# Optimization experiments

Hardware: AMD Instinct MI355X
Metric: run time of the kernel (lower is better)

## Reference

```python
import jax, jax.numpy as jnp
import numpy as np
from jax import lax

B, L, NCH, NQ, NL, FW, NCLS = 256, 3000, 4, 8, 2, 128, 5
BN_EPS = 1e-5


def setup_inputs() -> dict:
    key = jax.random.key(0)
    ks = jax.random.split(key, 24)
    rn = lambda k, shape, s=0.05: jax.random.normal(k, shape, jnp.float32) * s
    inp = {}
    inp['x'] = jax.random.normal(ks[0], (B, NCH, L), jnp.float32)
    inp['conv1_w'] = rn(ks[1], (32, NCH, 7)); inp['conv1_b'] = rn(ks[2], (32,))
    inp['bn1_g'] = 1.0 + rn(ks[3], (32,)); inp['bn1_b'] = rn(ks[3], (32,))
    inp['conv2_w'] = rn(ks[4], (64, 32, 7)); inp['conv2_b'] = rn(ks[5], (64,))
    inp['bn2_g'] = 1.0 + rn(ks[6], (64,)); inp['bn2_b'] = rn(ks[6], (64,))
    inp['conv3_w'] = rn(ks[7], (128, 64, 7)); inp['conv3_b'] = rn(ks[8], (128,))
    inp['bn3_g'] = 1.0 + rn(ks[9], (128,)); inp['bn3_b'] = rn(ks[9], (128,))
    inp['conv4_w'] = rn(ks[10], (128, 128, 7)); inp['conv4_b'] = rn(ks[11], (128,))
    inp['bn4_g'] = 1.0 + rn(ks[12], (128,)); inp['bn4_b'] = rn(ks[12], (128,))
    inp['fc_w'] = rn(ks[13], (FW, 128)); inp['fc_b'] = rn(ks[14], (FW,))
    inp['ang_w'] = rn(ks[15], (NQ, FW)); inp['ang_b'] = rn(ks[16], (NQ,))
    # TorchLayer default init: uniform in [0, 2*pi)
    inp['qw'] = jax.random.uniform(ks[17], (NL, NQ, 3), jnp.float32, 0.0, 2.0 * np.pi)
    inp['h1_w'] = rn(ks[18], (64, NQ)); inp['h1_b'] = rn(ks[19], (64,))
    inp['h2_w'] = rn(ks[20], (NCLS, 64)); inp['h2_b'] = rn(ks[21], (NCLS,))
    return inp


def _conv1d(x, w, b):
    y = lax.conv_general_dilated(x, w, (1,), [(3, 3)], dimension_numbers=('NCH', 'OIH', 'NCH'))
    return y + b[None, :, None]


def _bn(x, g, b):  # eval-mode BN: running_mean=0, running_var=1
    inv = 1.0 / np.sqrt(1.0 + BN_EPS)
    return x * (g * inv)[None, :, None] + b[None, :, None]


def _maxpool4(x):
    return lax.reduce_window(x, -jnp.inf, lax.max, (1, 1, 4), (1, 1, 4), 'VALID')


def _apply_1q(state, U, w, batched):
    # state: (B, 2**NQ); wire 0 = most significant bit (PennyLane convention)
    bs = state.shape[0]
    st = state.reshape(bs, 2 ** w, 2, -1)
    if batched:
        new = jnp.einsum('sab,slbr->slar', U, st)
    else:
        new = jnp.einsum('ab,slbr->slar', U, st)
    return new.reshape(bs, -1)


def _apply_cnot(state, c, t):
    bs = state.shape[0]
    q1, q2 = min(c, t), max(c, t)
    s = state.reshape(bs, 2 ** q1, 2, 2 ** (q2 - q1 - 1), 2, -1)
    ci, ti = (2, 4) if c < t else (4, 2)
    c0 = lax.index_in_dim(s, 0, ci, keepdims=True)
    c1 = jnp.flip(lax.index_in_dim(s, 1, ci, keepdims=True), axis=ti)
    return jnp.concatenate([c0, c1], axis=ci).reshape(bs, -1)


def _rot_matrix(phi, th, om):
    # PennyLane Rot(phi, theta, omega) = RZ(omega) RY(theta) RZ(phi)
    cm, sm = jnp.cos(th / 2), jnp.sin(th / 2)
    m00 = jnp.exp(-0.5j * (phi + om)) * cm
    m01 = -jnp.exp(0.5j * (phi - om)) * sm
    m10 = jnp.exp(-0.5j * (phi - om)) * sm
    m11 = jnp.exp(0.5j * (phi + om)) * cm
    return jnp.stack([jnp.stack([m00, m01]), jnp.stack([m10, m11])]).astype(jnp.complex64)


def _qsim(angles, qw):
    bs = angles.shape[0]
    dim = 2 ** NQ
    state = jnp.zeros((bs, dim), jnp.complex64).at[:, 0].set(1.0)
    # AngleEmbedding: RY(angle_w) on each wire (batched matrices)
    c, s = jnp.cos(angles / 2), jnp.sin(angles / 2)
    for w in range(NQ):
        U = jnp.stack([jnp.stack([c[:, w], -s[:, w]], -1),
                       jnp.stack([s[:, w], c[:, w]], -1)], -2).astype(jnp.complex64)
        state = _apply_1q(state, U, w, batched=True)
    # StronglyEntanglingLayers: Rot on each wire, then CNOT ring with range r
    for l in range(NL):
        for w in range(NQ):
            U = _rot_matrix(qw[l, w, 0], qw[l, w, 1], qw[l, w, 2])
            state = _apply_1q(state, U, w, batched=False)
        r = (l % (NQ - 1)) + 1
        for i in range(NQ):
            state = _apply_cnot(state, i, (i + r) % NQ)
    probs = state.real ** 2 + state.imag ** 2
    z = [probs.reshape(bs, 2 ** w, 2, -1)[:, :, 0].sum((1, 2))
         - probs.reshape(bs, 2 ** w, 2, -1)[:, :, 1].sum((1, 2)) for w in range(NQ)]
    return jnp.stack(z, -1)  # (B, NQ)


def reference(x, conv1_w, conv1_b, bn1_g, bn1_b, conv2_w, conv2_b, bn2_g, bn2_b,
              conv3_w, conv3_b, bn3_g, bn3_b, conv4_w, conv4_b, bn4_g, bn4_b,
              fc_w, fc_b, ang_w, ang_b, qw, h1_w, h1_b, h2_w, h2_b):
    h = jax.nn.relu(_bn(_conv1d(x, conv1_w, conv1_b), bn1_g, bn1_b))
    h = jax.nn.relu(_bn(_conv1d(h, conv2_w, conv2_b), bn2_g, bn2_b))
    h = _maxpool4(h)
    h = jax.nn.relu(_bn(_conv1d(h, conv3_w, conv3_b), bn3_g, bn3_b))
    h = _maxpool4(h)
    h = jax.nn.relu(_bn(_conv1d(h, conv4_w, conv4_b), bn4_g, bn4_b))
    h = h.mean(-1)  # AdaptiveAvgPool1d(1) + Flatten -> (B, 128)
    h = jax.nn.relu(h @ fc_w.T + fc_b)  # Dropout is identity in eval
    raw = h @ ang_w.T + ang_b
    angles = np.pi * jnp.tanh(raw)
    q = _qsim(angles, qw)
    h2 = jax.nn.relu(q @ h1_w.T + h1_b)
    return h2 @ h2_w.T + h2_b
```

## Files before the change

kernel.cpp:

```cpp
#include <hip/hip_runtime.h>
#include <hip/hip_bf16.h>

#define BN_INV 0.9999950000375f
#define PI_F   3.14159265358979f

typedef __attribute__((ext_vector_type(8))) short s16x8;
typedef __attribute__((ext_vector_type(4))) float f32x4;
typedef __attribute__((ext_vector_type(4))) unsigned short u16x4;

__device__ inline unsigned short f2bf(float f) {
  union { float f; unsigned u; } v; v.f = f;
  unsigned r = v.u + 0x7fffu + ((v.u >> 16) & 1u);
  return (unsigned short)(r >> 16);
}

__global__ __launch_bounds__(256) void k_pack(
    const float* __restrict__ w1, const float* __restrict__ w2,
    const float* __restrict__ w3, const float* __restrict__ w4,
    unsigned short* __restrict__ w1p, unsigned short* __restrict__ w2p,
    unsigned short* __restrict__ w3p, unsigned short* __restrict__ w4p,
    float* __restrict__ h4)
{
  int e = blockIdx.x * 256 + threadIdx.x;
  if (e < 2048) {
    int co = e >> 6, k = e & 63, kk = k >> 3, ci = k & 7;
    w1p[e] = (ci < 4 && kk < 7) ? f2bf(w1[co * 28 + ci * 7 + kk]) : (unsigned short)0;
  } else if (e < 16384) {
    int t = e - 2048; int co = t / 224, k = t % 224, kk = k >> 5, ci = k & 31;
    w2p[t] = f2bf(w2[co * 224 + ci * 7 + kk]);
  } else if (e < 73728) {
    int t = e - 16384; int co = t / 448, k = t % 448, kk = k >> 6, ci = k & 63;
    w3p[t] = f2bf(w3[co * 448 + ci * 7 + kk]);
  } else if (e < 188416) {
    int t = e - 73728; int co = t / 896, k = t % 896, kk = k >> 7, ci = k & 127;
    w4p[t] = f2bf(w4[co * 896 + ci * 7 + kk]);
  } else if (e < 221184) {
    h4[e - 188416] = 0.f;
  }
}

__global__ __launch_bounds__(256) void k_conv1(
    const float* __restrict__ x, const unsigned short* __restrict__ w1p,
    const float* __restrict__ cb, const float* __restrict__ bng,
    const float* __restrict__ bnb, unsigned short* __restrict__ h1t)
{
  __shared__ __align__(16) char lds[520 * 16 + 4096 + 256];
  float* scs = (float*)(lds + 520 * 16 + 4096);
  const int tid = threadIdx.x;
  const int b = blockIdx.y;
  const int l0 = blockIdx.x * 512;

  for (int r = tid; r < 519; r += 256) {
    int gr = l0 + r - 3;
    s16x8 v;
    if (gr >= 0 && gr < 3000) {
      const float* xr = x + b * 4 * 3000 + gr;
      v[0] = (short)f2bf(xr[0]);
      v[1] = (short)f2bf(xr[3000]);
      v[2] = (short)f2bf(xr[6000]);
      v[3] = (short)f2bf(xr[9000]);
      v[4] = 0; v[5] = 0; v[6] = 0; v[7] = 0;
    } else {
      for (int i = 0; i < 8; ++i) v[i] = 0;
    }
    *(s16x8*)(lds + r * 16) = v;
  }
  {
    int co = tid >> 3, c = tid & 7;
    s16x8 v = *(const s16x8*)(w1p + co * 64 + c * 8);
    *(s16x8*)(lds + 8320 + ((co * 128 + c * 16) ^ ((co & 7) << 4))) = v;
  }
  if (tid < 32) {
    float sc = bng[tid] * BN_INV;
    scs[tid * 2] = sc;
    scs[tid * 2 + 1] = fmaf(cb[tid], sc, bnb[tid]);
  }
  __syncthreads();

  const int w = tid >> 6, l = tid & 63, lr = l & 15, g = l >> 4;
  const int wp = w * 128;
  f32x4 acc[2][8];
  for (int m = 0; m < 2; ++m)
    for (int n = 0; n < 8; ++n)
      for (int i = 0; i < 4; ++i) acc[m][n][i] = 0.f;

  #pragma unroll
  for (int s = 0; s < 2; ++s) {
    s16x8 a[2], bf[8];
    #pragma unroll
    for (int m = 0; m < 2; ++m) {
      int co = m * 16 + lr;
      a[m] = *(const s16x8*)(lds + 8320 + ((co * 128 + s * 64 + g * 16) ^ ((co & 7) << 4)));
    }
    #pragma unroll
    for (int n = 0; n < 8; ++n) {
      int row = wp + n * 16 + lr + s * 4 + g;
      bf[n] = *(const s16x8*)(lds + row * 16);
    }
    #pragma unroll
    for (int m = 0; m < 2; ++m)
      #pragma unroll
      for (int n = 0; n < 8; ++n)
        acc[m][n] = __builtin_amdgcn_mfma_f32_16x16x32_bf16(a[m], bf[n], acc[m][n], 0, 0, 0);
  }

  #pragma unroll
  for (int m = 0; m < 2; ++m) {
    int co0 = m * 16 + g * 4;
    float sc[4], sh[4];
    #pragma unroll
    for (int j = 0; j < 4; ++j) { sc[j] = scs[(co0 + j) * 2]; sh[j] = scs[(co0 + j) * 2 + 1]; }
    #pragma unroll
    for (int n = 0; n < 8; ++n) {
      int gp = l0 + wp + n * 16 + lr;
      if (gp < 3000) {
        u16x4 o;
        #pragma unroll
        for (int j = 0; j < 4; ++j)
          o[j] = f2bf(fmaxf(fmaf(acc[m][n][j], sc[j], sh[j]), 0.f));
        *(u16x4*)(h1t + (b * 3000 + gp) * 32 + co0) = o;
      }
    }
  }
}

__global__ __launch_bounds__(256) void k_conv2(
    const unsigned short* __restrict__ h1t, const unsigned short* __restrict__ w2p,
    const float* __restrict__ cb, const float* __restrict__ bng,
    const float* __restrict__ bnb, unsigned short* __restrict__ h2pt)
{
  __shared__ __align__(16) char lds[264 * 64 + 28672 + 512];
  float* scs = (float*)(lds + 264 * 64 + 28672);
  const int tid = threadIdx.x, b = blockIdx.y;
  const int l0 = blockIdx.x * 256;

  for (int e = tid; e < 1048; e += 256) {
    int r = e >> 2, c = e & 3;
    int gr = l0 + r - 3;
    s16x8 v;
    if (gr >= 0 && gr < 3000) v = *(const s16x8*)(h1t + (b * 3000 + gr) * 32 + c * 8);
    else for (int i = 0; i < 8; ++i) v[i] = 0;
    *(s16x8*)(lds + ((r * 64 + c * 16) ^ ((r & 7) << 4))) = v;
  }
  for (int e = tid; e < 1792; e += 256) {
    int co = e / 28, c = e % 28;
    s16x8 v = *(const s16x8*)(w2p + co * 224 + c * 8);
    *(s16x8*)(lds + 16896 + ((co * 448 + c * 16) ^ ((co & 7) << 4))) = v;
  }
  if (tid < 64) {
    float sc = bng[tid] * BN_INV;
    scs[tid * 2] = sc;
    scs[tid * 2 + 1] = fmaf(cb[tid], sc, bnb[tid]);
  }
  __syncthreads();

  const int w = tid >> 6, l = tid & 63, lr = l & 15, g = l >> 4;
  const int wp = w * 64;
  f32x4 acc[4][4];
  for (int m = 0; m < 4; ++m)
    for (int n = 0; n < 4; ++n)
      for (int i = 0; i < 4; ++i) acc[m][n][i] = 0.f;

  #pragma unroll
  for (int s = 0; s < 7; ++s) {
    s16x8 a[4], bf[4];
    #pragma unroll
    for (int m = 0; m < 4; ++m) {
      int co = m * 16 + lr;
      a[m] = *(const s16x8*)(lds + 16896 + ((co * 448 + s * 64 + g * 16) ^ ((co & 7) << 4)));
    }
    #pragma unroll
    for (int n = 0; n < 4; ++n) {
      int row = wp + n * 16 + lr + s;
      bf[n] = *(const s16x8*)(lds + ((row * 64 + g * 16) ^ ((row & 7) << 4)));
    }
    #pragma unroll
    for (int m = 0; m < 4; ++m)
      #pragma unroll
      for (int n = 0; n < 4; ++n)
        acc[m][n] = __builtin_amdgcn_mfma_f32_16x16x32_bf16(a[m], bf[n], acc[m][n], 0, 0, 0);
  }

  #pragma unroll
  for (int m = 0; m < 4; ++m) {
    int co0 = m * 16 + g * 4;
    float sc[4], sh[4];
    #pragma unroll
    for (int j = 0; j < 4; ++j) { sc[j] = scs[(co0 + j) * 2]; sh[j] = scs[(co0 + j) * 2 + 1]; }
    #pragma unroll
    for (int n = 0; n < 4; ++n) {
      u16x4 o;
      #pragma unroll
      for (int j = 0; j < 4; ++j) {
        float t = fmaxf(fmaf(acc[m][n][j], sc[j], sh[j]), 0.f);
        float t1 = fmaxf(t, __shfl_xor(t, 1));
        float t2 = fmaxf(t1, __shfl_xor(t1, 2));
        o[j] = f2bf(t2);
      }
      int pp = (l0 + wp + n * 16 + lr) >> 2;
      if ((l & 3) == 0 && pp < 750)
        *(u16x4*)(h2pt + (b * 750 + pp) * 64 + co0) = o;
    }
  }
}

__global__ __launch_bounds__(256) void k_conv3(
    const unsigned short* __restrict__ h2pt, const unsigned short* __restrict__ w3p,
    const float* __restrict__ cb, const float* __restrict__ bng,
    const float* __restrict__ bnb, unsigned short* __restrict__ h3pt)
{
  __shared__ __align__(16) char lds[136 * 128 + 28672 + 512];
  float* scs = (float*)(lds + 136 * 128 + 28672);
  const int tid = threadIdx.x, b = blockIdx.y;
  const int tile = blockIdx.x >> 1, ch = blockIdx.x & 1;
  const int l0 = tile * 128, cg0 = ch * 64;

  for (int e = tid; e < 1072; e += 256) {
    int r = e >> 3, c = e & 7;
    int gr = l0 + r - 3;
    s16x8 v;
    if (gr >= 0 && gr < 750) v = *(const s16x8*)(h2pt + (b * 750 + gr) * 64 + c * 8);
    else for (int i = 0; i < 8; ++i) v[i] = 0;
    *(s16x8*)(lds + ((r * 128 + c * 16) ^ ((r & 7) << 4))) = v;
  }
  if (tid < 64) {
    int co = cg0 + tid;
    float sc = bng[co] * BN_INV;
    scs[tid * 2] = sc;
    scs[tid * 2 + 1] = fmaf(cb[co], sc, bnb[co]);
  }

  const int w = tid >> 6, l = tid & 63, lr = l & 15, g = l >> 4;
  const int wp = w * 32;
  f32x4 acc[4][2];
  for (int m = 0; m < 4; ++m)
    for (int n = 0; n < 2; ++n)
      for (int i = 0; i < 4; ++i) acc[m][n][i] = 0.f;

  for (int chunk = 0; chunk < 2; ++chunk) {
    __syncthreads();
    for (int e = tid; e < 1792; e += 256) {
      int co = e / 28, c = e % 28;
      s16x8 v = *(const s16x8*)(w3p + (cg0 + co) * 448 + chunk * 224 + c * 8);
      *(s16x8*)(lds + 17408 + ((co * 448 + c * 16) ^ ((co & 7) << 4))) = v;
    }
    __syncthreads();
    #pragma unroll
    for (int sl = 0; sl < 7; ++sl) {
      int k0 = chunk * 224 + sl * 32;
      int kk = k0 >> 6, cib = k0 & 63;
      s16x8 a[4], bf[2];
      #pragma unroll
      for (int m = 0; m < 4; ++m) {
        int co = m * 16 + lr;
        a[m] = *(const s16x8*)(lds + 17408 + ((co * 448 + sl * 64 + g * 16) ^ ((co & 7) << 4)));
      }
      #pragma unroll
      for (int n = 0; n < 2; ++n) {
        int row = wp + n * 16 + lr + kk;
        bf[n] = *(const s16x8*)(lds + ((row * 128 + cib * 2 + g * 16) ^ ((row & 7) << 4)));
      }
      #pragma unroll
      for (int m = 0; m < 4; ++m)
        #pragma unroll
        for (int n = 0; n < 2; ++n)
          acc[m][n] = __builtin_amdgcn_mfma_f32_16x16x32_bf16(a[m], bf[n], acc[m][n], 0, 0, 0);
    }
  }

  #pragma unroll
  for (int m = 0; m < 4; ++m) {
    int co0 = m * 16 + g * 4;
    float sc[4], sh[4];
    #pragma unroll
    for (int j = 0; j < 4; ++j) { sc[j] = scs[(co0 + j) * 2]; sh[j] = scs[(co0 + j) * 2 + 1]; }
    #pragma unroll
    for (int n = 0; n < 2; ++n) {
      u16x4 o;
      #pragma unroll
      for (int j = 0; j < 4; ++j) {
        float t = fmaxf(fmaf(acc[m][n][j], sc[j], sh[j]), 0.f);
        float t1 = fmaxf(t, __shfl_xor(t, 1));
        float t2 = fmaxf(t1, __shfl_xor(t1, 2));
        o[j] = f2bf(t2);
      }
      int pp = (l0 + wp + n * 16 + lr) >> 2;
      if ((l & 3) == 0 && pp < 187)
        *(u16x4*)(h3pt + (b * 187 + pp) * 128 + cg0 + co0) = o;
    }
  }
}

__global__ __launch_bounds__(256) void k_conv4(
    const unsigned short* __restrict__ h3pt, const unsigned short* __restrict__ w4p,
    const float* __restrict__ cb, const float* __restrict__ bng,
    const float* __restrict__ bnb, float* __restrict__ h4)
{
  __shared__ __align__(16) char lds[72 * 256 + 28672 + 512];
  float* scs = (float*)(lds + 72 * 256 + 28672);
  const int tid = threadIdx.x, b = blockIdx.y;
  const int ch = blockIdx.x & 1, pt = blockIdx.x >> 1;
  const int cg0 = ch * 64, p0 = pt * 64;

  for (int e = tid; e < 1120; e += 256) {
    int r = e >> 4, c = e & 15;
    int gr = p0 + r - 3;
    s16x8 v;
    if (gr >= 0 && gr < 187) v = *(const s16x8*)(h3pt + (b * 187 + gr) * 128 + c * 8);
    else for (int i = 0; i < 8; ++i) v[i] = 0;
    *(s16x8*)(lds + ((r * 256 + c * 16) ^ ((r & 7) << 4))) = v;
  }
  if (tid < 64) {
    int co = cg0 + tid;
    float sc = bng[co] * BN_INV;
    scs[tid * 2] = sc;
    scs[tid * 2 + 1] = fmaf(cb[co], sc, bnb[co]);
  }

  const int w = tid >> 6, l = tid & 63, lr = l & 15, g = l >> 4;
  const int co_off = (w & 1) * 32, pos_off = (w >> 1) * 32;
  f32x4 acc[2][2];
  for (int m = 0; m < 2; ++m)
    for (int n = 0; n < 2; ++n)
      for (int i = 0; i < 4; ++i) acc[m][n][i] = 0.f;

  for (int chunk = 0; chunk < 4; ++chunk) {
    __syncthreads();
    for (int e = tid; e < 1792; e += 256) {
      int co = e / 28, c = e % 28;
      s16x8 v = *(const s16x8*)(w4p + (cg0 + co) * 896 + chunk * 224 + c * 8);
      *(s16x8*)(lds + 18432 + ((co * 448 + c * 16) ^ ((co & 7) << 4))) = v;
    }
    __syncthreads();
    #pragma unroll
    for (int sl = 0; sl < 7; ++sl) {
      int k0 = chunk * 224 + sl * 32;
      int kk = k0 >> 7, cib = k0 & 127;
      s16x8 a[2], bf[2];
      #pragma unroll
      for (int m = 0; m < 2; ++m) {
        int co = co_off + m * 16 + lr;
        a[m] = *(const s16x8*)(lds + 18432 + ((co * 448 + sl * 64 + g * 16) ^ ((co & 7) << 4)));
      }
      #pragma unroll
      for (int n = 0; n < 2; ++n) {
        int row = pos_off + n * 16 + lr + kk;
        bf[n] = *(const s16x8*)(lds + ((row * 256 + cib * 2 + g * 16) ^ ((row & 7) << 4)));
      }
      #pragma unroll
      for (int m = 0; m < 2; ++m)
        #pragma unroll
        for (int n = 0; n < 2; ++n)
          acc[m][n] = __builtin_amdgcn_mfma_f32_16x16x32_bf16(a[m], bf[n], acc[m][n], 0, 0, 0);
    }
  }

  float psum[2][4];
  for (int m = 0; m < 2; ++m)
    for (int j = 0; j < 4; ++j) psum[m][j] = 0.f;
  #pragma unroll
  for (int m = 0; m < 2; ++m) {
    int col = co_off + m * 16 + g * 4;
    #pragma unroll
    for (int n = 0; n < 2; ++n) {
      int pos_g = p0 + pos_off + n * 16 + lr;
      #pragma unroll
      for (int j = 0; j < 4; ++j) {
        float t = fmaxf(fmaf(acc[m][n][j], scs[(col + j) * 2], scs[(col + j) * 2 + 1]), 0.f);
        if (pos_g < 187) psum[m][j] += t;
      }
    }
  }
  #pragma unroll
  for (int m = 0; m < 2; ++m)
    #pragma unroll
    for (int j = 0; j < 4; ++j) {
      float v = psum[m][j];
      v += __shfl_xor(v, 1);
      v += __shfl_xor(v, 2);
      v += __shfl_xor(v, 4);
      v += __shfl_xor(v, 8);
      if (lr == 0)
        atomicAdd(&h4[b * 128 + cg0 + co_off + m * 16 + g * 4 + j], v);
    }
}

__global__ __launch_bounds__(256) void k_head(
    const float* __restrict__ h4, const float* __restrict__ fc_w,
    const float* __restrict__ fc_b, const float* __restrict__ ang_w,
    const float* __restrict__ ang_b, const float* __restrict__ qw,
    const float* __restrict__ h1_w, const float* __restrict__ h1_b,
    const float* __restrict__ h2_w, const float* __restrict__ h2_b,
    float* __restrict__ out)
{
  __shared__ float hvec[128], fvec[128];
  __shared__ float rc[8], rs[8];
  __shared__ float rotm[16][8];
  __shared__ float2 st[256];
  __shared__ float parr[256];
  __shared__ float zv[8];
  __shared__ float hh[64];

  const int tid = threadIdx.x;
  const int b = blockIdx.x;

  if (tid < 128) hvec[tid] = h4[b * 128 + tid] * (1.0f / 187.0f);
  __syncthreads();

  if (tid < 128) {
    float a = fc_b[tid];
    const float* wr = fc_w + tid * 128;
    for (int k = 0; k < 128; ++k) a = fmaf(hvec[k], wr[k], a);
    fvec[tid] = fmaxf(a, 0.f);
  }
  __syncthreads();

  if (tid < 8) {
    float a = ang_b[tid];
    const float* wr = ang_w + tid * 128;
    for (int k = 0; k < 128; ++k) a = fmaf(fvec[k], wr[k], a);
    float ang = PI_F * tanhf(a);
    rc[tid] = cosf(0.5f * ang);
    rs[tid] = sinf(0.5f * ang);
  }
  if (tid >= 32 && tid < 48) {
    int g = tid - 32;
    float phi = qw[g * 3 + 0], th = qw[g * 3 + 1], om = qw[g * 3 + 2];
    float cm = cosf(0.5f * th), sm = sinf(0.5f * th);
    float a = 0.5f * (phi + om), bb = 0.5f * (phi - om);
    float ca = cosf(a), sa = sinf(a), cbb = cosf(bb), sbb = sinf(bb);
    rotm[g][0] =  cm * ca;  rotm[g][1] = -cm * sa;
    rotm[g][2] = -sm * cbb; rotm[g][3] = -sm * sbb;
    rotm[g][4] =  sm * cbb; rotm[g][5] = -sm * sbb;
    rotm[g][6] =  cm * ca;  rotm[g][7] =  cm * sa;
  }
  st[tid] = make_float2(tid == 0 ? 1.f : 0.f, 0.f);
  __syncthreads();

  for (int w = 0; w < 8; ++w) {
    if (tid < 128) {
      int bit = 7 - w;
      int i0 = ((tid >> bit) << (bit + 1)) | (tid & ((1 << bit) - 1));
      int i1 = i0 | (1 << bit);
      float c = rc[w], s = rs[w];
      float2 a0 = st[i0], a1 = st[i1];
      st[i0] = make_float2(c * a0.x - s * a1.x, c * a0.y - s * a1.y);
      st[i1] = make_float2(s * a0.x + c * a1.x, s * a0.y + c * a1.y);
    }
    __syncthreads();
  }

  for (int lay = 0; lay < 2; ++lay) {
    for (int w = 0; w < 8; ++w) {
      if (tid < 128) {
        int g = lay * 8 + w;
        int bit = 7 - w;
        int i0 = ((tid >> bit) << (bit + 1)) | (tid & ((1 << bit) - 1));
        int i1 = i0 | (1 << bit);
        float2 a0 = st[i0], a1 = st[i1];
        float2 n0, n1;
        n0.x = rotm[g][0] * a0.x - rotm[g][1] * a0.y + rotm[g][2] * a1.x - rotm[g][3] * a1.y;
        n0.y = rotm[g][0] * a0.y + rotm[g][1] * a0.x + rotm[g][2] * a1.y + rotm[g][3] * a1.x;
        n1.x = rotm[g][4] * a0.x - rotm[g][5] * a0.y + rotm[g][6] * a1.x - rotm[g][7] * a1.y;
        n1.y = rotm[g][4] * a0.y + rotm[g][5] * a0.x + rotm[g][6] * a1.y + rotm[g][7] * a1.x;
        st[i0] = n0;
        st[i1] = n1;
      }
      __syncthreads();
    }
    int r = (lay % 7) + 1;
    for (int i = 0; i < 8; ++i) {
      int c = i, t = (i + r) & 7;
      int cmask = 1 << (7 - c), tmask = 1 << (7 - t);
      int src = (tid & cmask) ? (tid ^ tmask) : tid;
      float2 v = st[src];
      __syncthreads();
      st[tid] = v;
      __syncthreads();
    }
  }

  parr[tid] = st[tid].x * st[tid].x + st[tid].y * st[tid].y;
  __syncthreads();
  if (tid < 8) {
    int bit = 7 - tid;
    float z = 0.f;
    for (int i = 0; i < 256; ++i)
      z += (i & (1 << bit)) ? -parr[i] : parr[i];
    zv[tid] = z;
  }
  __syncthreads();
  if (tid < 64) {
    float a = h1_b[tid];
    #pragma unroll
    for (int k = 0; k < 8; ++k) a = fmaf(zv[k], h1_w[tid * 8 + k], a);
    hh[tid] = fmaxf(a, 0.f);
  }
  __syncthreads();
  if (tid < 5) {
    float a = h2_b[tid];
    for (int j = 0; j < 64; ++j) a = fmaf(hh[j], h2_w[tid * 64 + j], a);
    out[b * 5 + tid] = a;
  }
}

extern "C" void kernel_launch(void* const* d_in, const int* in_sizes, int n_in,
                              void* d_out, int out_size, void* d_ws, size_t ws_size,
                              hipStream_t stream) {
  (void)in_sizes; (void)n_in; (void)out_size; (void)ws_size;
  const float* x    = (const float*)d_in[0];
  const float* c1w  = (const float*)d_in[1];
  const float* c1b  = (const float*)d_in[2];
  const float* b1g  = (const float*)d_in[3];
  const float* b1b  = (const float*)d_in[4];
  const float* c2w  = (const float*)d_in[5];
  const float* c2b  = (const float*)d_in[6];
  const float* b2g  = (const float*)d_in[7];
  const float* b2b  = (const float*)d_in[8];
  const float* c3w  = (const float*)d_in[9];
  const float* c3b  = (const float*)d_in[10];
  const float* b3g  = (const float*)d_in[11];
  const float* b3b  = (const float*)d_in[12];
  const float* c4w  = (const float*)d_in[13];
  const float* c4b  = (const float*)d_in[14];
  const float* b4g  = (const float*)d_in[15];
  const float* b4b  = (const float*)d_in[16];
  const float* fcw  = (const float*)d_in[17];
  const float* fcb  = (const float*)d_in[18];
  const float* angw = (const float*)d_in[19];
  const float* angb = (const float*)d_in[20];
  const float* qw   = (const float*)d_in[21];
  const float* h1w  = (const float*)d_in[22];
  const float* h1b  = (const float*)d_in[23];
  const float* h2w  = (const float*)d_in[24];
  const float* h2b  = (const float*)d_in[25];

  char* wsb = (char*)d_ws;
  unsigned short* w1p  = (unsigned short*)(wsb + 0);
  unsigned short* w2p  = (unsigned short*)(wsb + 4096);
  unsigned short* w3p  = (unsigned short*)(wsb + 32768);
  unsigned short* w4p  = (unsigned short*)(wsb + 147456);
  float*          h4   = (float*)(wsb + 393216);
  unsigned short* h1t  = (unsigned short*)(wsb + 1048576);
  unsigned short* h2pt = (unsigned short*)(wsb + 52428800);
  unsigned short* h3pt = (unsigned short*)(wsb + 79691776);

  k_pack<<<dim3(864), 256, 0, stream>>>(c1w, c2w, c3w, c4w, w1p, w2p, w3p, w4p, h4);
  k_conv1<<<dim3(6, 256),  256, 0, stream>>>(x, w1p, c1b, b1g, b1b, h1t);
  k_conv2<<<dim3(12, 256), 256, 0, stream>>>(h1t, w2p, c2b, b2g, b2b, h2pt);
  k_conv3<<<dim3(12, 256), 256, 0, stream>>>(h2pt, w3p, c3b, b3g, b3b, h3pt);
  k_conv4<<<dim3(6, 256),  256, 0, stream>>>(h3pt, w4p, c4b, b4g, b4b, h4);
  k_head<<<dim3(256), 256, 0, stream>>>(h4, fcw, fcb, angw, angb, qw,
                                        h1w, h1b, h2w, h2b, (float*)d_out);
}
```

Baseline: 251.4 us.

## Make conv2-4 persistent over tiles with register prefetch; warp-level quantum head

conv2 and conv3 now loop over several sequence tiles per block, keeping weights resident in LDS and prefetching the next input tile into registers during the MFMA work. conv4 covers all positions per block and double-buffers weight chunks through registers. The head kernel is rewritten as a single 64-lane wavefront that simulates the 8-qubit state in registers using shuffles instead of LDS plus barriers. The aim is to cut redundant weight loads, barrier and launch overhead, at the cost of much lower grid parallelism (fewer blocks) and higher register and LDS use.

```diff
diff --git a/kernel.cpp b/kernel.cpp
--- a/kernel.cpp
+++ b/kernel.cpp
@@ -129,19 +129,10 @@
     const float* __restrict__ cb, const float* __restrict__ bng,
     const float* __restrict__ bnb, unsigned short* __restrict__ h2pt)
 {
-  __shared__ __align__(16) char lds[264 * 64 + 28672 + 512];
-  float* scs = (float*)(lds + 264 * 64 + 28672);
-  const int tid = threadIdx.x, b = blockIdx.y;
-  const int l0 = blockIdx.x * 256;
-
-  for (int e = tid; e < 1048; e += 256) {
-    int r = e >> 2, c = e & 3;
-    int gr = l0 + r - 3;
-    s16x8 v;
-    if (gr >= 0 && gr < 3000) v = *(const s16x8*)(h1t + (b * 3000 + gr) * 32 + c * 8);
-    else for (int i = 0; i < 8; ++i) v[i] = 0;
-    *(s16x8*)(lds + ((r * 64 + c * 16) ^ ((r & 7) << 4))) = v;
-  }
+  __shared__ __align__(16) char lds[46080];
+  float* scs = (float*)(lds + 45568);
+  const int tid = threadIdx.x, b = blockIdx.y, bg = blockIdx.x;
+
   for (int e = tid; e < 1792; e += 256) {
     int co = e / 28, c = e % 28;
     s16x8 v = *(const s16x8*)(w2p + co * 224 + c * 8);
@@ -152,55 +143,102 @@
     scs[tid * 2] = sc;
     scs[tid * 2 + 1] = fmaf(cb[tid], sc, bnb[tid]);
   }
+  {
+    int l0 = bg * 1024;
+    #pragma unroll
+    for (int i = 0; i < 5; ++i) {
+      int e = tid + i * 256;
+      if (e < 1048) {
+        int r = e >> 2, c = e & 3, gr = l0 - 3 + r;
+        s16x8 v;
+        if (gr >= 0 && gr < 3000) v = *(const s16x8*)(h1t + (b * 3000 + gr) * 32 + c * 8);
+        else for (int q = 0; q < 8; ++q) v[q] = 0;
+        *(s16x8*)(lds + ((r * 64 + c * 16) ^ ((r & 7) << 4))) = v;
+      }
+    }
+  }
   __syncthreads();
 
   const int w = tid >> 6, l = tid & 63, lr = l & 15, g = l >> 4;
   const int wp = w * 64;
-  f32x4 acc[4][4];
-  for (int m = 0; m < 4; ++m)
-    for (int n = 0; n < 4; ++n)
-      for (int i = 0; i < 4; ++i) acc[m][n][i] = 0.f;
-
-  #pragma unroll
-  for (int s = 0; s < 7; ++s) {
-    s16x8 a[4], bf[4];
+
+  for (int t = 0; t < 4; ++t) {
+    const int l0 = bg * 1024 + t * 256;
+
+    s16x8 xr[5];
+    if (t < 3) {
+      int nl0 = l0 + 256;
+      #pragma unroll
+      for (int i = 0; i < 5; ++i) {
+        for (int q = 0; q < 8; ++q) xr[i][q] = 0;
+        int e = tid + i * 256;
+        if (e < 1048) {
+          int r = e >> 2, c = e & 3, gr = nl0 - 3 + r;
+          if (gr >= 0 && gr < 3000)
+            xr[i] = *(const s16x8*)(h1t + (b * 3000 + gr) * 32 + c * 8);
+        }
+      }
+    }
+
+    f32x4 acc[4][4];
+    for (int m = 0; m < 4; ++m)
+      for (int n = 0; n < 4; ++n)
+        for (int i = 0; i < 4; ++i) acc[m][n][i] = 0.f;
+
+    #pragma unroll
+    for (int s = 0; s < 7; ++s) {
+      s16x8 a[4], bf[4];
+      #pragma unroll
+      for (int m = 0; m < 4; ++m) {
+        int co = m * 16 + lr;
+        a[m] = *(const s16x8*)(lds + 16896 + ((co * 448 + s * 64 + g * 16) ^ ((co & 7) << 4)));
+      }
+      #pragma unroll
+      for (int n = 0; n < 4; ++n) {
+        int row = wp + n * 16 + lr + s;
+        bf[n] = *(const s16x8*)(lds + ((row * 64 + g * 16) ^ ((row & 7) << 4)));
+      }
+      #pragma unroll
+      for (int m = 0; m < 4; ++m)
+        #pragma unroll
+        for (int n = 0; n < 4; ++n)
+          acc[m][n] = __builtin_amdgcn_mfma_f32_16x16x32_bf16(a[m], bf[n], acc[m][n], 0, 0, 0);
+    }
+
     #pragma unroll
     for (int m = 0; m < 4; ++m) {
-      int co = m * 16 + lr;
-      a[m] = *(const s16x8*)(lds + 16896 + ((co * 448 + s * 64 + g * 16) ^ ((co & 7) << 4)));
-    }
-    #pragma unroll
-    for (int n = 0; n < 4; ++n) {
-      int row = wp + n * 16 + lr + s;
-      bf[n] = *(const s16x8*)(lds + ((row * 64 + g * 16) ^ ((row & 7) << 4)));
-    }
-    #pragma unroll
-    for (int m = 0; m < 4; ++m)
-      #pragma unroll
-      for (int n = 0; n < 4; ++n)
-        acc[m][n] = __builtin_amdgcn_mfma_f32_16x16x32_bf16(a[m], bf[n], acc[m][n], 0, 0, 0);
-  }
-
-  #pragma unroll
-  for (int m = 0; m < 4; ++m) {
-    int co0 = m * 16 + g * 4;
-    float sc[4], sh[4];
-    #pragma unroll
-    for (int j = 0; j < 4; ++j) { sc[j] = scs[(co0 + j) * 2]; sh[j] = scs[(co0 + j) * 2 + 1]; }
-    #pragma unroll
-    for (int n = 0; n < 4; ++n) {
-      u16x4 o;
-      #pragma unroll
-      for (int j = 0; j < 4; ++j) {
-        float t = fmaxf(fmaf(acc[m][n][j], sc[j], sh[j]), 0.f);
-        float t1 = fmaxf(t, __shfl_xor(t, 1));
-        float t2 = fmaxf(t1, __shfl_xor(t1, 2));
-        o[j] = f2bf(t2);
-      }
-      int pp = (l0 + wp + n * 16 + lr) >> 2;
-      if ((l & 3) == 0 && pp < 750)
-        *(u16x4*)(h2pt + (b * 750 + pp) * 64 + co0) = o;
-    }
+      int co0 = m * 16 + g * 4;
+      float sc[4], sh[4];
+      #pragma unroll
+      for (int j = 0; j < 4; ++j) { sc[j] = scs[(co0 + j) * 2]; sh[j] = scs[(co0 + j) * 2 + 1]; }
+      #pragma unroll
+      for (int n = 0; n < 4; ++n) {
+        u16x4 o;
+        #pragma unroll
+        for (int j = 0; j < 4; ++j) {
+          float tv = fmaxf(fmaf(acc[m][n][j], sc[j], sh[j]), 0.f);
+          float t1 = fmaxf(tv, __shfl_xor(tv, 1));
+          float t2 = fmaxf(t1, __shfl_xor(t1, 2));
+          o[j] = f2bf(t2);
+        }
+        int pp = (l0 + wp + n * 16 + lr) >> 2;
+        if ((l & 3) == 0 && pp < 750)
+          *(u16x4*)(h2pt + (b * 750 + pp) * 64 + co0) = o;
+      }
+    }
+
+    __syncthreads();
+    if (t < 3) {
+      #pragma unroll
+      for (int i = 0; i < 5; ++i) {
+        int e = tid + i * 256;
+        if (e < 1048) {
+          int r = e >> 2, c = e & 3;
+          *(s16x8*)(lds + ((r * 64 + c * 16) ^ ((r & 7) << 4))) = xr[i];
+        }
+      }
+    }
+    __syncthreads();
   }
 }
 
@@ -209,19 +247,15 @@
     const float* __restrict__ cb, const float* __restrict__ bng,
     const float* __restrict__ bnb, unsigned short* __restrict__ h3pt)
 {
-  __shared__ __align__(16) char lds[136 * 128 + 28672 + 512];
-  float* scs = (float*)(lds + 136 * 128 + 28672);
-  const int tid = threadIdx.x, b = blockIdx.y;
-  const int tile = blockIdx.x >> 1, ch = blockIdx.x & 1;
-  const int l0 = tile * 128, cg0 = ch * 64;
-
-  for (int e = tid; e < 1072; e += 256) {
-    int r = e >> 3, c = e & 7;
-    int gr = l0 + r - 3;
-    s16x8 v;
-    if (gr >= 0 && gr < 750) v = *(const s16x8*)(h2pt + (b * 750 + gr) * 64 + c * 8);
-    else for (int i = 0; i < 8; ++i) v[i] = 0;
-    *(s16x8*)(lds + ((r * 128 + c * 16) ^ ((r & 7) << 4))) = v;
+  __shared__ __align__(16) char lds[75776];
+  float* scs = (float*)(lds + 74752);
+  const int tid = threadIdx.x, b = blockIdx.y, ch = blockIdx.x;
+  const int cg0 = ch * 64;
+
+  for (int e = tid; e < 3584; e += 256) {
+    int co = e / 56, c = e % 56;
+    s16x8 v = *(const s16x8*)(w3p + (cg0 + co) * 448 + c * 8);
+    *(s16x8*)(lds + 17408 + ((co * 896 + c * 16) ^ ((co & 7) << 4))) = v;
   }
   if (tid < 64) {
     int co = cg0 + tid;
@@ -229,31 +263,55 @@
     scs[tid * 2] = sc;
     scs[tid * 2 + 1] = fmaf(cb[co], sc, bnb[co]);
   }
+  {
+    #pragma unroll
+    for (int i = 0; i < 5; ++i) {
+      int e = tid + i * 256;
+      if (e < 1072) {
+        int r = e >> 3, c = e & 7, gr = r - 3;
+        s16x8 v;
+        if (gr >= 0 && gr < 750) v = *(const s16x8*)(h2pt + (b * 750 + gr) * 64 + c * 8);
+        else for (int q = 0; q < 8; ++q) v[q] = 0;
+        *(s16x8*)(lds + ((r * 128 + c * 16) ^ ((r & 7) << 4))) = v;
+      }
+    }
+  }
+  __syncthreads();
 
   const int w = tid >> 6, l = tid & 63, lr = l & 15, g = l >> 4;
   const int wp = w * 32;
-  f32x4 acc[4][2];
-  for (int m = 0; m < 4; ++m)
-    for (int n = 0; n < 2; ++n)
-      for (int i = 0; i < 4; ++i) acc[m][n][i] = 0.f;
-
-  for (int chunk = 0; chunk < 2; ++chunk) {
-    __syncthreads();
-    for (int e = tid; e < 1792; e += 256) {
-      int co = e / 28, c = e % 28;
-      s16x8 v = *(const s16x8*)(w3p + (cg0 + co) * 448 + chunk * 224 + c * 8);
-      *(s16x8*)(lds + 17408 + ((co * 448 + c * 16) ^ ((co & 7) << 4))) = v;
-    }
-    __syncthreads();
-    #pragma unroll
-    for (int sl = 0; sl < 7; ++sl) {
-      int k0 = chunk * 224 + sl * 32;
-      int kk = k0 >> 6, cib = k0 & 63;
+
+  for (int t = 0; t < 6; ++t) {
+    const int l0 = t * 128;
+
+    s16x8 xr[5];
+    if (t < 5) {
+      int nl0 = l0 + 128;
+      #pragma unroll
+      for (int i = 0; i < 5; ++i) {
+        for (int q = 0; q < 8; ++q) xr[i][q] = 0;
+        int e = tid + i * 256;
+        if (e < 1072) {
+          int r = e >> 3, c = e & 7, gr = nl0 - 3 + r;
+          if (gr >= 0 && gr < 750)
+            xr[i] = *(const s16x8*)(h2pt + (b * 750 + gr) * 64 + c * 8);
+        }
+      }
+    }
+
+    f32x4 acc[4][2];
+    for (int m = 0; m < 4; ++m)
+      for (int n = 0; n < 2; ++n)
+        for (int i = 0; i < 4; ++i) acc[m][n][i] = 0.f;
+
+    #pragma unroll
+    for (int sl = 0; sl < 14; ++sl) {
+      int kk = sl >> 1, cib = (sl & 1) * 32;
       s16x8 a[4], bf[2];
       #pragma unroll
       for (int m = 0; m < 4; ++m) {
         int co = m * 16 + lr;
-        a[m] = *(const s16x8*)(lds + 17408 + ((co * 448 + sl * 64 + g * 16) ^ ((co & 7) << 4)));
+        a[m] = *(const s16x8*)(lds + 17408 + ((co * 896 + sl * 64 + g * 16) ^ ((co & 7) << 4)));
       }
       #pragma unroll
       for (int n = 0; n < 2; ++n) {
@@ -266,28 +324,41 @@
         for (int n = 0; n < 2; ++n)
           acc[m][n] = __builtin_amdgcn_mfma_f32_16x16x32_bf16(a[m], bf[n], acc[m][n], 0, 0, 0);
     }
-  }
-
-  #pragma unroll
-  for (int m = 0; m < 4; ++m) {
-    int co0 = m * 16 + g * 4;
-    float sc[4], sh[4];
-    #pragma unroll
-    for (int j = 0; j < 4; ++j) { sc[j] = scs[(co0 + j) * 2]; sh[j] = scs[(co0 + j) * 2 + 1]; }
-    #pragma unroll
-    for (int n = 0; n < 2; ++n) {
-      u16x4 o;
-      #pragma unroll
-      for (int j = 0; j < 4; ++j) {
-        float t = fmaxf(fmaf(acc[m][n][j], sc[j], sh[j]), 0.f);
-        float t1 = fmaxf(t, __shfl_xor(t, 1));
-        float t2 = fmaxf(t1, __shfl_xor(t1, 2));
-        o[j] = f2bf(t2);
-      }
-      int pp = (l0 + wp + n * 16 + lr) >> 2;
-      if ((l & 3) == 0 && pp < 187)
-        *(u16x4*)(h3pt + (b * 187 + pp) * 128 + cg0 + co0) = o;
-    }
+
+    #pragma unroll
+    for (int m = 0; m < 4; ++m) {
+      int co0 = m * 16 + g * 4;
+      float sc[4], sh[4];
+      #pragma unroll
+      for (int j = 0; j < 4; ++j) { sc[j] = scs[(co0 + j) * 2]; sh[j] = scs[(co0 + j) * 2 + 1]; }
+      #pragma unroll
+      for (int n = 0; n < 2; ++n) {
+        u16x4 o;
+        #pragma unroll
+        for (int j = 0; j < 4; ++j) {
+          float tv = fmaxf(fmaf(acc[m][n][j], sc[j], sh[j]), 0.f);
+          float t1 = fmaxf(tv, __shfl_xor(tv, 1));
+          float t2 = fmaxf(t1, __shfl_xor(t1, 2));
+          o[j] = f2bf(t2);
+        }
+        int pp = (l0 + wp + n * 16 + lr) >> 2;
+        if ((l & 3) == 0 && pp < 187)
+          *(u16x4*)(h3pt + (b * 187 + pp) * 128 + cg0 + co0) = o;
+      }
+    }
+
+    __syncthreads();
+    if (t < 5) {
+      #pragma unroll
+      for (int i = 0; i < 5; ++i) {
+        int e = tid + i * 256;
+        if (e < 1072) {
+          int r = e >> 3, c = e & 7;
+          *(s16x8*)(lds + ((r * 128 + c * 16) ^ ((r & 7) << 4))) = xr[i];
+        }
+      }
+    }
+    __syncthreads();
   }
 }
 
@@ -296,19 +367,26 @@
     const float* __restrict__ cb, const float* __restrict__ bng,
     const float* __restrict__ bnb, float* __restrict__ h4)
 {
-  __shared__ __align__(16) char lds[72 * 256 + 28672 + 512];
-  float* scs = (float*)(lds + 72 * 256 + 28672);
-  const int tid = threadIdx.x, b = blockIdx.y;
-  const int ch = blockIdx.x & 1, pt = blockIdx.x >> 1;
-  const int cg0 = ch * 64, p0 = pt * 64;
-
-  for (int e = tid; e < 1120; e += 256) {
-    int r = e >> 4, c = e & 15;
-    int gr = p0 + r - 3;
-    s16x8 v;
-    if (gr >= 0 && gr < 187) v = *(const s16x8*)(h3pt + (b * 187 + gr) * 128 + c * 8);
-    else for (int i = 0; i < 8; ++i) v[i] = 0;
-    *(s16x8*)(lds + ((r * 256 + c * 16) ^ ((r & 7) << 4))) = v;
+  __shared__ __align__(16) char lds[79872];
+  float* scs = (float*)(lds + 79360);
+  const int tid = threadIdx.x, b = blockIdx.y, ch = blockIdx.x;
+  const int cg0 = ch * 64;
+
+  #pragma unroll
+  for (int i = 0; i < 13; ++i) {
+    int e = tid + i * 256;
+    if (e < 3168) {
+      int r = e >> 4, c = e & 15, gr = r - 3;
+      s16x8 v;
+      if (gr >= 0 && gr < 187) v = *(const s16x8*)(h3pt + (b * 187 + gr) * 128 + c * 8);
+      else for (int q = 0; q < 8; ++q) v[q] = 0;
+      *(s16x8*)(lds + ((r * 256 + c * 16) ^ ((r & 7) << 4))) = v;
+    }
+  }
+  for (int e = tid; e < 1792; e += 256) {
+    int co = e / 28, c = e % 28;
+    s16x8 v = *(const s16x8*)(w4p + (cg0 + co) * 896 + c * 8);
+    *(s16x8*)(lds + 50688 + ((co * 448 + c * 16) ^ ((co & 7) << 4))) = v;
   }
   if (tid < 64) {
     int co = cg0 + tid;
@@ -316,43 +394,57 @@
     scs[tid * 2] = sc;
     scs[tid * 2 + 1] = fmaf(cb[co], sc, bnb[co]);
   }
+  __syncthreads();
 
   const int w = tid >> 6, l = tid & 63, lr = l & 15, g = l >> 4;
-  const int co_off = (w & 1) * 32, pos_off = (w >> 1) * 32;
-  f32x4 acc[2][2];
+  const int co_off = (w & 1) * 32, pos_off = (w >> 1) * 96;
+
+  f32x4 acc[2][6];
   for (int m = 0; m < 2; ++m)
-    for (int n = 0; n < 2; ++n)
+    for (int n = 0; n < 6; ++n)
       for (int i = 0; i < 4; ++i) acc[m][n][i] = 0.f;
 
   for (int chunk = 0; chunk < 4; ++chunk) {
-    __syncthreads();
-    for (int e = tid; e < 1792; e += 256) {
-      int co = e / 28, c = e % 28;
-      s16x8 v = *(const s16x8*)(w4p + (cg0 + co) * 896 + chunk * 224 + c * 8);
-      *(s16x8*)(lds + 18432 + ((co * 448 + c * 16) ^ ((co & 7) << 4))) = v;
-    }
-    __syncthreads();
+    s16x8 wr[7];
+    if (chunk < 3) {
+      #pragma unroll
+      for (int i = 0; i < 7; ++i) {
+        int e = tid + i * 256;
+        int co = e / 28, c = e % 28;
+        wr[i] = *(const s16x8*)(w4p + (cg0 + co) * 896 + (chunk + 1) * 224 + c * 8);
+      }
+    }
     #pragma unroll
     for (int sl = 0; sl < 7; ++sl) {
       int k0 = chunk * 224 + sl * 32;
       int kk = k0 >> 7, cib = k0 & 127;
-      s16x8 a[2], bf[2];
+      s16x8 a[2], bf[6];
       #pragma unroll
       for (int m = 0; m < 2; ++m) {
         int co = co_off + m * 16 + lr;
-        a[m] = *(const s16x8*)(lds + 18432 + ((co * 448 + sl * 64 + g * 16) ^ ((co & 7) << 4)));
-      }
-      #pragma unroll
-      for (int n = 0; n < 2; ++n) {
+        a[m] = *(const s16x8*)(lds + 50688 + ((co * 448 + sl * 64 + g * 16) ^ ((co & 7) << 4)));
+      }
+      #pragma unroll
+      for (int n = 0; n < 6; ++n) {
         int row = pos_off + n * 16 + lr + kk;
         bf[n] = *(const s16x8*)(lds + ((row * 256 + cib * 2 + g * 16) ^ ((row & 7) << 4)));
       }
       #pragma unroll
       for (int m = 0; m < 2; ++m)
         #pragma unroll
-        for (int n = 0; n < 2; ++n)
+        for (int n = 0; n < 6; ++n)
           acc[m][n] = __builtin_amdgcn_mfma_f32_16x16x32_bf16(a[m], bf[n], acc[m][n], 0, 0, 0);
     }
+    __syncthreads();
+    if (chunk < 3) {
+      #pragma unroll
+      for (int i = 0; i < 7; ++i) {
+        int e = tid + i * 256;
+        int co = e / 28, c = e % 28;
+        *(s16x8*)(lds + 50688 + ((co * 448 + c * 16) ^ ((co & 7) << 4))) = wr[i];
+      }
+    }
+    __syncthreads();
   }
 
   float psum[2][4];
@@ -362,12 +454,12 @@
   for (int m = 0; m < 2; ++m) {
     int col = co_off + m * 16 + g * 4;
     #pragma unroll
-    for (int n = 0; n < 2; ++n) {
-      int pos_g = p0 + pos_off + n * 16 + lr;
+    for (int n = 0; n < 6; ++n) {
+      int pos_g = pos_off + n * 16 + lr;
       #pragma unroll
       for (int j = 0; j < 4; ++j) {
-        float t = fmaxf(fmaf(acc[m][n][j], scs[(col + j) * 2], scs[(col + j) * 2 + 1]), 0.f);
-        if (pos_g < 187) psum[m][j] += t;
+        float tv = fmaxf(fmaf(acc[m][n][j], scs[(col + j) * 2], scs[(col + j) * 2 + 1]), 0.f);
+        if (pos_g < 187) psum[m][j] += tv;
       }
     }
   }
@@ -385,7 +477,7 @@
     }
 }
 
-__global__ __launch_bounds__(256) void k_head(
+__global__ __launch_bounds__(64) void k_head(
     const float* __restrict__ h4, const float* __restrict__ fc_w,
     const float* __restrict__ fc_b, const float* __restrict__ ang_w,
     const float* __restrict__ ang_b, const float* __restrict__ qw,
@@ -393,115 +485,207 @@
     const float* __restrict__ h2_w, const float* __restrict__ h2_b,
     float* __restrict__ out)
 {
-  __shared__ float hvec[128], fvec[128];
-  __shared__ float rc[8], rs[8];
-  __shared__ float rotm[16][8];
-  __shared__ float2 st[256];
-  __shared__ float parr[256];
-  __shared__ float zv[8];
-  __shared__ float hh[64];
-
-  const int tid = threadIdx.x;
+  const int lane = threadIdx.x;
   const int b = blockIdx.x;
 
-  if (tid < 128) hvec[tid] = h4[b * 128 + tid] * (1.0f / 187.0f);
-  __syncthreads();
-
-  if (tid < 128) {
-    float a = fc_b[tid];
-    const float* wr = fc_w + tid * 128;
-    for (int k = 0; k < 128; ++k) a = fmaf(hvec[k], wr[k], a);
-    fvec[tid] = fmaxf(a, 0.f);
-  }
-  __syncthreads();
-
-  if (tid < 8) {
-    float a = ang_b[tid];
-    const float* wr = ang_w + tid * 128;
-    for (int k = 0; k < 128; ++k) a = fmaf(fvec[k], wr[k], a);
-    float ang = PI_F * tanhf(a);
-    rc[tid] = cosf(0.5f * ang);
-    rs[tid] = sinf(0.5f * ang);
-  }
-  if (tid >= 32 && tid < 48) {
-    int g = tid - 32;
-    float phi = qw[g * 3 + 0], th = qw[g * 3 + 1], om = qw[g * 3 + 2];
+  float hv0 = h4[b * 128 + lane] * (1.0f / 187.0f);
+  float hv1 = h4[b * 128 + 64 + lane] * (1.0f / 187.0f);
+
+  float a0 = fc_b[lane], a1 = fc_b[lane + 64];
+  {
+    const float* w0 = fc_w + lane * 128;
+    const float* w1 = fc_w + (lane + 64) * 128;
+    #pragma unroll
+    for (int k = 0; k < 64; ++k) {
+      float hk = __shfl(hv0, k);
+      a0 = fmaf(hk, w0[k], a0);
+      a1 = fmaf(hk, w1[k], a1);
+    }
+    #pragma unroll
+    for (int k = 0; k < 64; ++k) {
+      float hk = __shfl(hv1, k);
+      a0 = fmaf(hk, w0[64 + k], a0);
+      a1 = fmaf(hk, w1[64 + k], a1);
+    }
+  }
+  float f0 = fmaxf(a0, 0.f), f1 = fmaxf(a1, 0.f);
+
+  float rcw[8], rsw[8];
+  #pragma unroll
+  for (int o = 0; o < 8; ++o) {
+    float p = fmaf(f0, ang_w[o * 128 + lane], f1 * ang_w[o * 128 + 64 + lane]);
+    #pragma unroll
+    for (int m = 1; m < 64; m <<= 1) p += __shfl_xor(p, m);
+    float aa = PI_F * tanhf(ang_b[o] + p);
+    rcw[o] = cosf(0.5f * aa);
+    rsw[o] = sinf(0.5f * aa);
+  }
+
+  float r0, r1, r2, r3, r4, r5, r6, r7;
+  {
+    int gq = lane & 15;
+    float phi = qw[gq * 3], th = qw[gq * 3 + 1], om = qw[gq * 3 + 2];
     float cm = cosf(0.5f * th), sm = sinf(0.5f * th);
-    float a = 0.5f * (phi + om), bb = 0.5f * (phi - om);
-    float ca = cosf(a), sa = sinf(a), cbb = cosf(bb), sbb = sinf(bb);
-    rotm[g][0] =  cm * ca;  rotm[g][1] = -cm * sa;
-    rotm[g][2] = -sm * cbb; rotm[g][3] = -sm * sbb;
-    rotm[g][4] =  sm * cbb; rotm[g][5] = -sm * sbb;
-    rotm[g][6] =  cm * ca;  rotm[g][7] =  cm * sa;
-  }
-  st[tid] = make_float2(tid == 0 ? 1.f : 0.f, 0.f);
-  __syncthreads();
-
-  for (int w = 0; w < 8; ++w) {
-    if (tid < 128) {
-      int bit = 7 - w;
-      int i0 = ((tid >> bit) << (bit + 1)) | (tid & ((1 << bit) - 1));
-      int i1 = i0 | (1 << bit);
-      float c = rc[w], s = rs[w];
-      float2 a0 = st[i0], a1 = st[i1];
-      st[i0] = make_float2(c * a0.x - s * a1.x, c * a0.y - s * a1.y);
-      st[i1] = make_float2(s * a0.x + c * a1.x, s * a0.y + c * a1.y);
-    }
-    __syncthreads();
-  }
-
+    float ap = 0.5f * (phi + om), bm = 0.5f * (phi - om);
+    float ca = cosf(ap), sa = sinf(ap), cb2 = cosf(bm), sb2 = sinf(bm);
+    r0 = cm * ca;   r1 = -cm * sa;
+    r2 = -sm * cb2; r3 = -sm * sb2;
+    r4 = sm * cb2;  r5 = -sm * sb2;
+    r6 = cm * ca;   r7 = cm * sa;
+  }
+
+  float2 st[4];
+  st[0] = make_float2((lane == 0) ? 1.f : 0.f, 0.f);
+  st[1] = make_float2(0.f, 0.f);
+  st[2] = make_float2(0.f, 0.f);
+  st[3] = make_float2(0.f, 0.f);
+
+  auto ry_lane = [&](int lx, float c, float s) {
+    #pragma unroll
+    for (int j = 0; j < 4; ++j) {
+      float ox = __shfl_xor(st[j].x, lx);
+      float oy = __shfl_xor(st[j].y, lx);
+      bool hi = (lane & lx) != 0;
+      float a0x = hi ? ox : st[j].x, a0y = hi ? oy : st[j].y;
+      float a1x = hi ? st[j].x : ox, a1y = hi ? st[j].y : oy;
+      float cA = hi ? s : c, cB = hi ? c : -s;
+      st[j].x = cA * a0x + cB * a1x;
+      st[j].y = cA * a0y + cB * a1y;
+    }
+  };
+#define RY_SLOT(J0, J1, c, s) { \
+    float2 A = st[J0], B = st[J1]; \
+    st[J0].x = (c) * A.x - (s) * B.x; st[J0].y = (c) * A.y - (s) * B.y; \
+    st[J1].x = (s) * A.x + (c) * B.x; st[J1].y = (s) * A.y + (c) * B.y; }
+
+  ry_lane(32, rcw[0], rsw[0]);
+  ry_lane(16, rcw[1], rsw[1]);
+  ry_lane(8,  rcw[2], rsw[2]);
+  ry_lane(4,  rcw[3], rsw[3]);
+  ry_lane(2,  rcw[4], rsw[4]);
+  ry_lane(1,  rcw[5], rsw[5]);
+  RY_SLOT(0, 2, rcw[6], rsw[6]); RY_SLOT(1, 3, rcw[6], rsw[6]);
+  RY_SLOT(0, 1, rcw[7], rsw[7]); RY_SLOT(2, 3, rcw[7], rsw[7]);
+
+  auto rot_lane = [&](int gi, int lx) {
+    float m00x = __shfl(r0, gi), m00y = __shfl(r1, gi);
+    float m01x = __shfl(r2, gi), m01y = __shfl(r3, gi);
+    float m10x = __shfl(r4, gi), m10y = __shfl(r5, gi);
+    float m11x = __shfl(r6, gi), m11y = __shfl(r7, gi);
+    #pragma unroll
+    for (int j = 0; j < 4; ++j) {
+      float ox = __shfl_xor(st[j].x, lx);
+      float oy = __shfl_xor(st[j].y, lx);
+      bool hi = (lane & lx) != 0;
+      float a0x = hi ? ox : st[j].x, a0y = hi ? oy : st[j].y;
+      float a1x = hi ? st[j].x : ox, a1y = hi ? st[j].y : oy;
+      float cx = hi ? m10x : m00x, cy = hi ? m10y : m00y;
+      float dx = hi ? m11x : m01x, dy = hi ? m11y : m01y;
+      st[j].x = cx * a0x - cy * a0y + dx * a1x - dy * a1y;
+      st[j].y = cx * a0y + cy * a0x + dx * a1y + dy * a1x;
+    }
+  };
+#define ROT_SLOT(J0, J1) { \
+    float2 A = st[J0], B = st[J1]; \
+    st[J0].x = m00x * A.x - m00y * A.y + m01x * B.x - m01y * B.y; \
+    st[J0].y = m00x * A.y + m00y * A.x + m01x * B.y + m01y * B.x; \
+    st[J1].x = m10x * A.x - m10y * A.y + m11x * B.x - m11y * B.y; \
+    st[J1].y = m10x * A.y + m10y * A.x + m11x * B.y + m11y * B.x; }
+  auto rot_slot = [&](int gi, int bit) {
+    float m00x = __shfl(r0, gi), m00y = __shfl(r1, gi);
+    float m01x = __shfl(r2, gi), m01y = __shfl(r3, gi);
+    float m10x = __shfl(r4, gi), m10y = __shfl(r5, gi);
+    float m11x = __shfl(r6, gi), m11y = __shfl(r7, gi);
+    if (bit == 1) { ROT_SLOT(0, 2) ROT_SLOT(1, 3) }
+    else          { ROT_SLOT(0, 1) ROT_SLOT(2, 3) }
+  };
+
+  auto cnot = [&](int cmask, int tmask) {
+    bool cb0, cb1, cb2, cb3;
+    if (cmask >= 4) {
+      bool cbl = (lane & (cmask >> 2)) != 0;
+      cb0 = cbl; cb1 = cbl; cb2 = cbl; cb3 = cbl;
+    } else {
+      cb0 = false;
+      cb1 = (1 & cmask) != 0;
+      cb2 = (2 & cmask) != 0;
+      cb3 = (3 & cmask) != 0;
+    }
+    if (tmask >= 4) {
+      int lx = tmask >> 2;
+      { float ox = __shfl_xor(st[0].x, lx), oy = __shfl_xor(st[0].y, lx); if (cb0) { st[0].x = ox; st[0].y = oy; } }
+      { float ox = __shfl_xor(st[1].x, lx), oy = __shfl_xor(st[1].y, lx); if (cb1) { st[1].x = ox; st[1].y = oy; } }
+      { float ox = __shfl_xor(st[2].x, lx), oy = __shfl_xor(st[2].y, lx); if (cb2) { st[2].x = ox; st[2].y = oy; } }
+      { float ox = __shfl_xor(st[3].x, lx), oy = __shfl_xor(st[3].y, lx); if (cb3) { st[3].x = ox; st[3].y = oy; } }
+    } else {
+      float2 o0 = st[0], o1 = st[1], o2 = st[2], o3 = st[3];
+      if (tmask == 2) {
+        if (cb0) st[0] = o2;
+        if (cb1) st[1] = o3;
+        if (cb2) st[2] = o0;
+        if (cb3) st[3] = o1;
+      } else {
+        if (cb0) st[0] = o1;
+        if (cb1) st[1] = o0;
+        if (cb2) st[2] = o3;
+        if (cb3) st[3] = o2;
+      }
+    }
+  };
+
+  #pragma unroll
   for (int lay = 0; lay < 2; ++lay) {
-    for (int w = 0; w < 8; ++w) {
-      if (tid < 128) {
-        int g = lay * 8 + w;
-        int bit = 7 - w;
-        int i0 = ((tid >> bit) << (bit + 1)) | (tid & ((1 << bit) - 1));
-        int i1 = i0 | (1 << bit);
-        float2 a0 = st[i0], a1 = st[i1];
-        float2 n0, n1;
-        n0.x = rotm[g][0] * a0.x - rotm[g][1] * a0.y + rotm[g][2] * a1.x - rotm[g][3] * a1.y;
-        n0.y = rotm[g][0] * a0.y + rotm[g][1] * a0.x + rotm[g][2] * a1.y + rotm[g][3] * a1.x;
-        n1.x = rotm[g][4] * a0.x - rotm[g][5] * a0.y + rotm[g][6] * a1.x - rotm[g][7] * a1.y;
-        n1.y = rotm[g][4] * a0.y + rotm[g][5] * a0.x + rotm[g][6] * a1.y + rotm[g][7] * a1.x;
-        st[i0] = n0;
-        st[i1] = n1;
-      }
-      __syncthreads();
-    }
-    int r = (lay % 7) + 1;
+    rot_lane(lay * 8 + 0, 32);
+    rot_lane(lay * 8 + 1, 16);
+    rot_lane(lay * 8 + 2, 8);
+    rot_lane(lay * 8 + 3, 4);
+    rot_lane(lay * 8 + 4, 2);
+    rot_lane(lay * 8 + 5, 1);
+    rot_slot(lay * 8 + 6, 1);
+    rot_slot(lay * 8 + 7, 0);
+    int r = lay + 1;
+    #pragma unroll
     for (int i = 0; i < 8; ++i) {
       int c = i, t = (i + r) & 7;
-      int cmask = 1 << (7 - c), tmask = 1 << (7 - t);
-      int src = (tid & cmask) ? (tid ^ tmask) : tid;
-      float2 v = st[src];
-      __syncthreads();
-      st[tid] = v;
-      __syncthreads();
-    }
-  }
-
-  parr[tid] = st[tid].x * st[tid].x + st[tid].y * st[tid].y;
-  __syncthreads();
-  if (tid < 8) {
-    int bit = 7 - tid;
-    float z = 0.f;
-    for (int i = 0; i < 256; ++i)
-      z += (i & (1 << bit)) ? -parr[i] : parr[i];
-    zv[tid] = z;
-  }
-  __syncthreads();
-  if (tid < 64) {
-    float a = h1_b[tid];
-    #pragma unroll
-    for (int k = 0; k < 8; ++k) a = fmaf(zv[k], h1_w[tid * 8 + k], a);
-    hh[tid] = fmaxf(a, 0.f);
-  }
-  __syncthreads();
-  if (tid < 5) {
-    float a = h2_b[tid];
-    for (int j = 0; j < 64; ++j) a = fmaf(hh[j], h2_w[tid * 64 + j], a);
-    out[b * 5 + tid] = a;
-  }
+      cnot(1 << (7 - c), 1 << (7 - t));
+    }
+  }
+
+  float p0 = st[0].x * st[0].x + st[0].y * st[0].y;
+  float p1 = st[1].x * st[1].x + st[1].y * st[1].y;
+  float p2 = st[2].x * st[2].x + st[2].y * st[2].y;
+  float p3 = st[3].x * st[3].x + st[3].y * st[3].y;
+  float sAll = p0 + p1 + p2 + p3;
+  float zp[8];
+  zp[0] = (lane & 32) ? -sAll : sAll;
+  zp[1] = (lane & 16) ? -sAll : sAll;
+  zp[2] = (lane & 8)  ? -sAll : sAll;
+  zp[3] = (lane & 4)  ? -sAll : sAll;
+  zp[4] = (lane & 2)  ? -sAll : sAll;
+  zp[5] = (lane & 1)  ? -sAll : sAll;
+  zp[6] = (p0 + p1) - (p2 + p3);
+  zp[7] = (p0 - p1) + (p2 - p3);
+  #pragma unroll
+  for (int o = 0; o < 8; ++o) {
+    #pragma unroll
+    for (int m = 1; m < 64; m <<= 1) zp[o] += __shfl_xor(zp[o], m);
+  }
+
+  float ah = h1_b[lane];
+  const float* hw = h1_w + lane * 8;
+  #pragma unroll
+  for (int k = 0; k < 8; ++k) ah = fmaf(zp[k], hw[k], ah);
+  float hh = fmaxf(ah, 0.f);
+
+  #pragma unroll
+  for (int o = 0; o < 5; ++o) {
+    float v = hh * h2_w[o * 64 + lane];
+    #pragma unroll
+    for (int m = 1; m < 64; m <<= 1) v += __shfl_xor(v, m);
+    if (lane == 0) out[b * 5 + o] = v + h2_b[o];
+  }
+#undef RY_SLOT
+#undef ROT_SLOT
 }
 
 extern "C" void kernel_launch(void* const* d_in, const int* in_sizes, int n_in,
@@ -546,10 +730,10 @@
   unsigned short* h3pt = (unsigned short*)(wsb + 79691776);
 
   k_pack<<<dim3(864), 256, 0, stream>>>(c1w, c2w, c3w, c4w, w1p, w2p, w3p, w4p, h4);
-  k_conv1<<<dim3(6, 256),  256, 0, stream>>>(x, w1p, c1b, b1g, b1b, h1t);
-  k_conv2<<<dim3(12, 256), 256, 0, stream>>>(h1t, w2p, c2b, b2g, b2b, h2pt);
-  k_conv3<<<dim3(12, 256), 256, 0, stream>>>(h2pt, w3p, c3b, b3g, b3b, h3pt);
-  k_conv4<<<dim3(6, 256),  256, 0, stream>>>(h3pt, w4p, c4b, b4g, b4b, h4);
-  k_head<<<dim3(256), 256, 0, stream>>>(h4, fcw, fcb, angw, angb, qw,
-                                        h1w, h1b, h2w, h2b, (float*)d_out);
+  k_conv1<<<dim3(6, 256), 256, 0, stream>>>(x, w1p, c1b, b1g, b1b, h1t);
+  k_conv2<<<dim3(3, 256), 256, 0, stream>>>(h1t, w2p, c2b, b2g, b2b, h2pt);
+  k_conv3<<<dim3(2, 256), 256, 0, stream>>>(h2pt, w3p, c3b, b3g, b3b, h3pt);
+  k_conv4<<<dim3(2, 256), 256, 0, stream>>>(h3pt, w4p, c4b, b4g, b4b, h4);
+  k_head<<<dim3(256), 64, 0, stream>>>(h4, fcw, fcb, angw, angb, qw,
+                                       h1w, h1b, h2w, h2b, (float*)d_out);
 }
```

Measured after the change: 251.9 us. Within noise of the previous version (+0.2%).
